# Kernel tuning notes

Hardware: AMD Instinct MI355X
Metric: run time of the kernel (lower is better)

The kernel has to match this reference:

```python
import jax, jax.numpy as jnp
import numpy as np

B, T, D, F, E, K = 2, 1024, 1024, 2048, 8, 2

def setup_inputs() -> dict:
    key = jax.random.key(0)
    ks = jax.random.split(key, 9)
    s = 0.02
    return {
        "states": jax.random.normal(ks[0], (B, T, D), dtype=jnp.float32),
        "Wg": jax.random.normal(ks[1], (D, E), dtype=jnp.float32) * s,
        "W_in": jax.random.normal(ks[2], (E, D, F), dtype=jnp.float32) * s,
        "b_in": jnp.zeros((E, F), dtype=jnp.float32),
        "W_scale": jax.random.normal(ks[3], (E, D, F), dtype=jnp.float32) * s,
        "b_scale": jnp.zeros((E, F), dtype=jnp.float32),
        "W_out": jax.random.normal(ks[4], (E, F, D), dtype=jnp.float32) * s,
        "b_out": jnp.zeros((E, D), dtype=jnp.float32),
        "num_selected": K,
    }

def reference(states, Wg, W_in, b_in, W_scale, b_scale, W_out, b_out, num_selected):
    b, t, d = states.shape
    x = states.reshape(-1, d)                      # [N, D]
    n = x.shape[0]
    # router: softmax over experts, then top-k + renormalize
    probs = jax.nn.softmax(x @ Wg, axis=-1)        # [N, E]
    topw, topi = jax.lax.top_k(probs, num_selected)  # [N, K]
    topw = topw / topw.sum(axis=-1, keepdims=True)
    # dense combine weights [N, E]: zero except selected experts
    w_full = jnp.zeros_like(probs).at[jnp.arange(n)[:, None], topi].set(topw)
    # gated-GELU expert MLPs, batched over experts
    h = jnp.einsum('nd,edf->enf', x, W_in) + b_in[:, None, :]       # [E, N, F]
    s = jnp.einsum('nd,edf->enf', x, W_scale) + b_scale[:, None, :]
    inner = jax.nn.gelu(h, approximate=False) * s                    # exact GELU (torch default)
    y = jnp.einsum('enf,efd->end', inner, W_out) + b_out[:, None, :]  # [E, N, D]
    out = jnp.einsum('end,ne->nd', y, w_full)                         # weighted combine
    return out.reshape(b, t, d)
```

## Files before the change

### kernel.cpp

```cpp
#include <hip/hip_runtime.h>
#include <hip/hip_bf16.h>
#include <math.h>

#define N_TOK 2048
#define DIM   1024
#define FF    2048
#define NEXP  8
#define NSLOT (N_TOK * 2)

typedef __attribute__((ext_vector_type(8))) short short8;
typedef __attribute__((ext_vector_type(4))) float f32x4;
typedef _Float16 half_t;
typedef __attribute__((ext_vector_type(4))) _Float16 h16x4;

__device__ __forceinline__ unsigned short f2bf(float f) {
    unsigned int u = __float_as_uint(f);
    u += 0x7FFFu + ((u >> 16) & 1u);
    return (unsigned short)(u >> 16);
}

#define GLOAD_LDS16(g, l) \
    __builtin_amdgcn_global_load_lds((const __attribute__((address_space(1))) unsigned int*)(g), \
                                     (__attribute__((address_space(3))) unsigned int*)(l), 16, 0, 0)

__global__ __launch_bounds__(256) void k_router(const float* __restrict__ x,
        const float* __restrict__ Wg, int* __restrict__ hdr,
        int* __restrict__ tok_e, float* __restrict__ tok_w) {
    int wave = threadIdx.x >> 6, lane = threadIdx.x & 63;
    int t = blockIdx.x * 4 + wave;
    float acc[NEXP];
#pragma unroll
    for (int e = 0; e < NEXP; ++e) acc[e] = 0.f;
    const float* xr = x + (size_t)t * DIM;
    for (int d = lane; d < DIM; d += 64) {
        float xv = xr[d];
        const float* wr = Wg + d * NEXP;
#pragma unroll
        for (int e = 0; e < NEXP; ++e) acc[e] += xv * wr[e];
    }
#pragma unroll
    for (int off = 32; off > 0; off >>= 1) {
#pragma unroll
        for (int e = 0; e < NEXP; ++e) acc[e] += __shfl_down(acc[e], off);
    }
    if (lane == 0) {
        int e0 = 0;
#pragma unroll
        for (int e = 1; e < NEXP; ++e) if (acc[e] > acc[e0]) e0 = e;
        int e1 = -1;
#pragma unroll
        for (int e = 0; e < NEXP; ++e) {
            if (e == e0) continue;
            if (e1 < 0 || acc[e] > acc[e1]) e1 = e;
        }
        float w0 = 1.f / (1.f + expf(acc[e1] - acc[e0]));
        tok_e[2 * t] = e0; tok_e[2 * t + 1] = e1;
        tok_w[2 * t] = w0; tok_w[2 * t + 1] = 1.f - w0;
        atomicAdd(&hdr[e0], 1);
        atomicAdd(&hdr[e1], 1);
    }
}

__global__ void k_scan(int* hdr) {
    if (threadIdx.x == 0 && blockIdx.x == 0) {
        int s = 0;
        for (int e = 0; e < NEXP; ++e) {
            hdr[16 + e] = s;
            hdr[8 + e]  = s;
            s += hdr[e];
        }
        hdr[24] = s;
    }
}

__global__ __launch_bounds__(256) void k_assign(const float* __restrict__ x,
        int* __restrict__ hdr, const int* __restrict__ tok_e,
        int* __restrict__ tok_slot, unsigned short* __restrict__ xg) {
    __shared__ int sh[2];
    int t = blockIdx.x;
    if (threadIdx.x == 0) {
        int e0 = tok_e[2 * t], e1 = tok_e[2 * t + 1];
        int p0 = atomicAdd(&hdr[8 + e0], 1);
        int p1 = atomicAdd(&hdr[8 + e1], 1);
        tok_slot[2 * t] = p0; tok_slot[2 * t + 1] = p1;
        sh[0] = p0; sh[1] = p1;
    }
    __syncthreads();
    int s0 = sh[0], s1 = sh[1];
    const float4* xr = (const float4*)(x + (size_t)t * DIM);
    float4 v = xr[threadIdx.x];
    ushort4 b;
    b.x = f2bf(v.x); b.y = f2bf(v.y); b.z = f2bf(v.z); b.w = f2bf(v.w);
    ((ushort4*)(xg + (size_t)s0 * DIM))[threadIdx.x] = b;
    ((ushort4*)(xg + (size_t)s1 * DIM))[threadIdx.x] = b;
}

__global__ __launch_bounds__(256) void k_cvt(
        const float* __restrict__ s0, const float* __restrict__ s1,
        const float* __restrict__ s2, unsigned short* __restrict__ d0,
        unsigned short* __restrict__ d1, unsigned short* __restrict__ d2) {
    int bz = blockIdx.y;
    int which = bz >> 3, e = bz & 7;
    int R = (which == 2) ? FF : DIM;
    int C = (which == 2) ? DIM : FF;
    const float* S = ((which == 0) ? s0 : (which == 1) ? s1 : s2) + (size_t)e * DIM * FF;
    unsigned short* D = ((which == 0) ? d0 : (which == 1) ? d1 : d2) + (size_t)e * DIM * FF;
    int tilesx = C >> 6;
    int tx = blockIdx.x % tilesx, ty = blockIdx.x / tilesx;
    int c0 = tx * 64, r0 = ty * 64;
    __shared__ unsigned short sh[64][65];
    int t = threadIdx.x;
    int rr = t >> 4, cc = (t & 15) * 4;
#pragma unroll
    for (int j = 0; j < 4; ++j) {
        int r = rr + j * 16;
        float4 v = *(const float4*)(S + (size_t)(r0 + r) * C + c0 + cc);
        sh[r][cc + 0] = f2bf(v.x);
        sh[r][cc + 1] = f2bf(v.y);
        sh[r][cc + 2] = f2bf(v.z);
        sh[r][cc + 3] = f2bf(v.w);
    }
    __syncthreads();
    int oc = t >> 2, orr = (t & 3) * 16;
    unsigned short tmp[16];
#pragma unroll
    for (int j = 0; j < 16; ++j) tmp[j] = sh[orr + j][oc];
    unsigned short* q = D + (size_t)(c0 + oc) * R + r0 + orr;
    *(uint4*)q       = *(uint4*)&tmp[0];
    *(uint4*)(q + 8) = *(uint4*)&tmp[8];
}

__global__ __launch_bounds__(256, 2) void k_expert_hs(
        const unsigned short* __restrict__ xg,
        const unsigned short* __restrict__ Wth,
        const unsigned short* __restrict__ Wts,
        const float* __restrict__ b_in, const float* __restrict__ b_sc,
        const int* __restrict__ hdr, unsigned short* __restrict__ inner) {
    int e = blockIdx.z;
    int cnt = hdr[e];
    int mtile = blockIdx.y;
    if (mtile * 128 >= cnt) return;
    int base = hdr[16 + e];
    int f0 = blockIdx.x * 128;

    __shared__ unsigned short As[128 * 32];
    __shared__ unsigned short Bh[128 * 32];
    __shared__ unsigned short Bs[128 * 32];

    int tid = threadIdx.x;
    int wave = tid >> 6, lane = tid & 63;
    int lr = lane & 15, lq = lane >> 4;
    int wm = (wave >> 1) * 64, wf = (wave & 1) * 64;

    f32x4 acch[4][4], accs[4][4];
#pragma unroll
    for (int mi = 0; mi < 4; ++mi)
#pragma unroll
        for (int fi = 0; fi < 4; ++fi) {
            acch[mi][fi] = (f32x4){0.f, 0.f, 0.f, 0.f};
            accs[mi][fi] = (f32x4){0.f, 0.f, 0.f, 0.f};
        }

    int swzc = (lane & 3) ^ ((lane >> 3) & 3);
    int goff = (lane >> 2) * DIM + swzc * 8;
    int rdo = lr * 32 + (lq ^ ((lr >> 1) & 3)) * 8;

    const unsigned short* Abase = xg  + (size_t)(base + mtile * 128) * DIM + goff;
    const unsigned short* Hbase = Wth + ((size_t)e * FF + f0) * DIM + goff;
    const unsigned short* Sbase = Wts + ((size_t)e * FF + f0) * DIM + goff;
    int p0 = wave * 32, p1 = wave * 32 + 16;

    for (int k0 = 0; k0 < DIM; k0 += 32) {
        __syncthreads();
        GLOAD_LDS16(Abase + (size_t)p0 * DIM + k0, &As[p0 * 32]);
        GLOAD_LDS16(Abase + (size_t)p1 * DIM + k0, &As[p1 * 32]);
        GLOAD_LDS16(Hbase + (size_t)p0 * DIM + k0, &Bh[p0 * 32]);
        GLOAD_LDS16(Hbase + (size_t)p1 * DIM + k0, &Bh[p1 * 32]);
        GLOAD_LDS16(Sbase + (size_t)p0 * DIM + k0, &Bs[p0 * 32]);
        GLOAD_LDS16(Sbase + (size_t)p1 * DIM + k0, &Bs[p1 * 32]);
        __syncthreads();

        short8 af[4], bhf[4], bsf[4];
#pragma unroll
        for (int mi = 0; mi < 4; ++mi)
            af[mi] = *(const short8*)&As[(wm + mi * 16) * 32 + rdo];
#pragma unroll
        for (int fi = 0; fi < 4; ++fi) {
            bhf[fi] = *(const short8*)&Bh[(wf + fi * 16) * 32 + rdo];
            bsf[fi] = *(const short8*)&Bs[(wf + fi * 16) * 32 + rdo];
        }
#pragma unroll
        for (int mi = 0; mi < 4; ++mi)
#pragma unroll
            for (int fi = 0; fi < 4; ++fi) {
                acch[mi][fi] = __builtin_amdgcn_mfma_f32_16x16x32_bf16(
                    af[mi], bhf[fi], acch[mi][fi], 0, 0, 0);
                accs[mi][fi] = __builtin_amdgcn_mfma_f32_16x16x32_bf16(
                    af[mi], bsf[fi], accs[mi][fi], 0, 0, 0);
            }
    }

#pragma unroll
    for (int fi = 0; fi < 4; ++fi) {
        int f = f0 + wf + fi * 16 + lr;
        float bi = b_in[e * FF + f];
        float bs2 = b_sc[e * FF + f];
#pragma unroll
        for (int mi = 0; mi < 4; ++mi) {
#pragma unroll
            for (int r = 0; r < 4; ++r) {
                int rl = wm + mi * 16 + lq * 4 + r;
                int grow = mtile * 128 + rl;
                if (grow < cnt) {
                    float h = acch[mi][fi][r] + bi;
                    float s = accs[mi][fi][r] + bs2;
                    float g = 0.5f * h * (1.f + erff(h * 0.70710678f));
                    inner[(size_t)(base + grow) * FF + f] = f2bf(g * s);
                }
            }
        }
    }
}

__global__ __launch_bounds__(256, 2) void k_expert_out(
        const unsigned short* __restrict__ inner,
        const unsigned short* __restrict__ Wto,
        const int* __restrict__ hdr, half_t* __restrict__ pbuf) {
    int e = blockIdx.z & 7;
    int ks = blockIdx.z >> 3;
    int cnt = hdr[e];
    int mtile = blockIdx.y;
    if (mtile * 128 >= cnt) return;
    int base = hdr[16 + e];
    int d0 = blockIdx.x * 256;

    __shared__ unsigned short As[128 * 32];
    __shared__ unsigned short Bt[256 * 32];

    int tid = threadIdx.x;
    int wave = tid >> 6, lane = tid & 63;
    int lr = lane & 15, lq = lane >> 4;
    int wm = (wave >> 1) * 64, wn = (wave & 1) * 128;

    f32x4 acc[4][8];
#pragma unroll
    for (int mi = 0; mi < 4; ++mi)
#pragma unroll
        for (int ni = 0; ni < 8; ++ni) acc[mi][ni] = (f32x4){0.f, 0.f, 0.f, 0.f};

    int swzc = (lane & 3) ^ ((lane >> 3) & 3);
    int goff = (lane >> 2) * FF + swzc * 8;
    int rdo = lr * 32 + (lq ^ ((lr >> 1) & 3)) * 8;

    const unsigned short* Abase = inner + (size_t)(base + mtile * 128) * FF + goff;
    const unsigned short* Bbase = Wto + ((size_t)e * DIM + d0) * FF + goff;
    int pa0 = wave * 32, pa1 = wave * 32 + 16;
    int pb0 = wave * 64;

    int kbeg = ks * (FF / 2), kend = kbeg + FF / 2;

    for (int k0 = kbeg; k0 < kend; k0 += 32) {
        __syncthreads();
        GLOAD_LDS16(Abase + (size_t)pa0 * FF + k0, &As[pa0 * 32]);
        GLOAD_LDS16(Abase + (size_t)pa1 * FF + k0, &As[pa1 * 32]);
#pragma unroll
        for (int j = 0; j < 4; ++j)
            GLOAD_LDS16(Bbase + (size_t)(pb0 + j * 16) * FF + k0, &Bt[(pb0 + j * 16) * 32]);
        __syncthreads();

        short8 af[4], bfm[8];
#pragma unroll
        for (int mi = 0; mi < 4; ++mi)
            af[mi] = *(const short8*)&As[(wm + mi * 16) * 32 + rdo];
#pragma unroll
        for (int ni = 0; ni < 8; ++ni)
            bfm[ni] = *(const short8*)&Bt[(wn + ni * 16) * 32 + rdo];
#pragma unroll
        for (int mi = 0; mi < 4; ++mi)
#pragma unroll
            for (int ni = 0; ni < 8; ++ni)
                acc[mi][ni] = __builtin_amdgcn_mfma_f32_16x16x32_bf16(
                    af[mi], bfm[ni], acc[mi][ni], 0, 0, 0);
    }

    half_t* P = pbuf + (size_t)ks * NSLOT * DIM;
#pragma unroll
    for (int ni = 0; ni < 8; ++ni) {
        int d = d0 + wn + ni * 16 + lr;
#pragma unroll
        for (int mi = 0; mi < 4; ++mi) {
#pragma unroll
            for (int r = 0; r < 4; ++r) {
                int rl = wm + mi * 16 + lq * 4 + r;
                int grow = mtile * 128 + rl;
                if (grow < cnt)
                    P[(size_t)(base + grow) * DIM + d] = (half_t)acc[mi][ni][r];
            }
        }
    }
}

__global__ __launch_bounds__(256) void k_combine(const half_t* __restrict__ pbuf,
        const int* __restrict__ tok_slot, const int* __restrict__ tok_e,
        const float* __restrict__ tok_w, const float* __restrict__ b_out,
        float* __restrict__ out) {
    int t = blockIdx.x;
    int d = threadIdx.x * 4;
    int s0 = tok_slot[2 * t], s1 = tok_slot[2 * t + 1];
    int e0 = tok_e[2 * t], e1 = tok_e[2 * t + 1];
    float w0 = tok_w[2 * t], w1 = tok_w[2 * t + 1];
    const half_t* pA = pbuf;
    const half_t* pB = pbuf + (size_t)NSLOT * DIM;
    h16x4 a0 = *(const h16x4*)&pA[(size_t)s0 * DIM + d];
    h16x4 a1 = *(const h16x4*)&pB[(size_t)s0 * DIM + d];
    h16x4 c0 = *(const h16x4*)&pA[(size_t)s1 * DIM + d];
    h16x4 c1 = *(const h16x4*)&pB[(size_t)s1 * DIM + d];
    float4 b0 = *(const float4*)&b_out[e0 * DIM + d];
    float4 b1 = *(const float4*)&b_out[e1 * DIM + d];
    float4 r;
    r.x = w0 * ((float)a0.x + (float)a1.x + b0.x) + w1 * ((float)c0.x + (float)c1.x + b1.x);
    r.y = w0 * ((float)a0.y + (float)a1.y + b0.y) + w1 * ((float)c0.y + (float)c1.y + b1.y);
    r.z = w0 * ((float)a0.z + (float)a1.z + b0.z) + w1 * ((float)c0.z + (float)c1.z + b1.z);
    r.w = w0 * ((float)a0.w + (float)a1.w + b0.w) + w1 * ((float)c0.w + (float)c1.w + b1.w);
    *(float4*)&out[(size_t)t * DIM + d] = r;
}

extern "C" void kernel_launch(void* const* d_in, const int* in_sizes, int n_in,
                              void* d_out, int out_size, void* d_ws, size_t ws_size,
                              hipStream_t stream) {
    (void)in_sizes; (void)n_in; (void)out_size; (void)ws_size;
    const float* x    = (const float*)d_in[0];
    const float* Wg   = (const float*)d_in[1];
    const float* Win  = (const float*)d_in[2];
    const float* b_in = (const float*)d_in[3];
    const float* Wsc  = (const float*)d_in[4];
    const float* b_sc = (const float*)d_in[5];
    const float* Wout = (const float*)d_in[6];
    const float* b_out= (const float*)d_in[7];
    float* out = (float*)d_out;

    char* ws = (char*)d_ws;
    int*   hdr      = (int*)ws;
    int*   tok_e    = (int*)(ws + 256);
    float* tok_w    = (float*)(ws + 16640);
    int*   tok_slot = (int*)(ws + 33024);
    unsigned short* xg    = (unsigned short*)(ws + 65792);
    unsigned short* inner = (unsigned short*)(ws + 65792 + 8388608);
    half_t* pbuf = (half_t*)(ws + 65792 + 8388608 + 16777216);
    unsigned short* wt_h = (unsigned short*)(ws + 65792 + 8388608 + 16777216 + 16777216);
    unsigned short* wt_s = wt_h + (size_t)NEXP * FF * DIM;
    unsigned short* wt_o = wt_s + (size_t)NEXP * FF * DIM;

    hipMemsetAsync(hdr, 0, 256, stream);
    k_cvt<<<dim3(512, 24), dim3(256), 0, stream>>>(Win, Wsc, Wout, wt_h, wt_s, wt_o);
    k_router<<<dim3(N_TOK / 4), dim3(256), 0, stream>>>(x, Wg, hdr, tok_e, tok_w);
    k_scan<<<dim3(1), dim3(64), 0, stream>>>(hdr);
    k_assign<<<dim3(N_TOK), dim3(256), 0, stream>>>(x, hdr, tok_e, tok_slot, xg);
    k_expert_hs<<<dim3(FF / 128, 16, NEXP), dim3(256), 0, stream>>>(xg, wt_h, wt_s, b_in, b_sc, hdr, inner);
    k_expert_out<<<dim3(DIM / 256, 16, NEXP * 2), dim3(256), 0, stream>>>(inner, wt_o, hdr, pbuf);
    k_combine<<<dim3(N_TOK), dim3(256), 0, stream>>>(pbuf, tok_slot, tok_e, tok_w, b_out, out);
}
```

Measured before the change: 457.3 us.

## Double-buffer LDS tiles in expert GEMM kernels to overlap loads with MFMA

Both expert GEMM kernels now use two LDS buffers per operand. The next K-slice is issued with global_load_lds before the current slice is computed, and one barrier per iteration replaces two. The aim is to hide global-memory latency behind MFMA work. LDS use doubles to about 48KB per block in each kernel, which may limit occupancy. The barrier alone may not guarantee the async LDS loads have completed, since no explicit vmcnt wait is added.

```diff
diff --git a/kernel.cpp b/kernel.cpp
--- a/kernel.cpp
+++ b/kernel.cpp
@@ -143,9 +143,9 @@
     int base = hdr[16 + e];
     int f0 = blockIdx.x * 128;
 
-    __shared__ unsigned short As[128 * 32];
-    __shared__ unsigned short Bh[128 * 32];
-    __shared__ unsigned short Bs[128 * 32];
+    __shared__ unsigned short As[2 * 128 * 32];
+    __shared__ unsigned short Bh[2 * 128 * 32];
+    __shared__ unsigned short Bs[2 * 128 * 32];
 
     int tid = threadIdx.x;
     int wave = tid >> 6, lane = tid & 63;
@@ -170,24 +170,36 @@
     const unsigned short* Sbase = Wts + ((size_t)e * FF + f0) * DIM + goff;
     int p0 = wave * 32, p1 = wave * 32 + 16;
 
-    for (int k0 = 0; k0 < DIM; k0 += 32) {
-        __syncthreads();
-        GLOAD_LDS16(Abase + (size_t)p0 * DIM + k0, &As[p0 * 32]);
-        GLOAD_LDS16(Abase + (size_t)p1 * DIM + k0, &As[p1 * 32]);
-        GLOAD_LDS16(Hbase + (size_t)p0 * DIM + k0, &Bh[p0 * 32]);
-        GLOAD_LDS16(Hbase + (size_t)p1 * DIM + k0, &Bh[p1 * 32]);
-        GLOAD_LDS16(Sbase + (size_t)p0 * DIM + k0, &Bs[p0 * 32]);
-        GLOAD_LDS16(Sbase + (size_t)p1 * DIM + k0, &Bs[p1 * 32]);
-        __syncthreads();
+    GLOAD_LDS16(Abase + (size_t)p0 * DIM, &As[p0 * 32]);
+    GLOAD_LDS16(Abase + (size_t)p1 * DIM, &As[p1 * 32]);
+    GLOAD_LDS16(Hbase + (size_t)p0 * DIM, &Bh[p0 * 32]);
+    GLOAD_LDS16(Hbase + (size_t)p1 * DIM, &Bh[p1 * 32]);
+    GLOAD_LDS16(Sbase + (size_t)p0 * DIM, &Bs[p0 * 32]);
+    GLOAD_LDS16(Sbase + (size_t)p1 * DIM, &Bs[p1 * 32]);
+    __syncthreads();
+
+    const int NSTEP = DIM / 32;
+    for (int t = 0; t < NSTEP; ++t) {
+        int co = (t & 1) * (128 * 32);
+        if (t + 1 < NSTEP) {
+            int no = ((t & 1) ^ 1) * (128 * 32);
+            int k1 = (t + 1) * 32;
+            GLOAD_LDS16(Abase + (size_t)p0 * DIM + k1, &As[no + p0 * 32]);
+            GLOAD_LDS16(Abase + (size_t)p1 * DIM + k1, &As[no + p1 * 32]);
+            GLOAD_LDS16(Hbase + (size_t)p0 * DIM + k1, &Bh[no + p0 * 32]);
+            GLOAD_LDS16(Hbase + (size_t)p1 * DIM + k1, &Bh[no + p1 * 32]);
+            GLOAD_LDS16(Sbase + (size_t)p0 * DIM + k1, &Bs[no + p0 * 32]);
+            GLOAD_LDS16(Sbase + (size_t)p1 * DIM + k1, &Bs[no + p1 * 32]);
+        }
 
         short8 af[4], bhf[4], bsf[4];
 #pragma unroll
         for (int mi = 0; mi < 4; ++mi)
-            af[mi] = *(const short8*)&As[(wm + mi * 16) * 32 + rdo];
+            af[mi] = *(const short8*)&As[co + (wm + mi * 16) * 32 + rdo];
 #pragma unroll
         for (int fi = 0; fi < 4; ++fi) {
-            bhf[fi] = *(const short8*)&Bh[(wf + fi * 16) * 32 + rdo];
-            bsf[fi] = *(const short8*)&Bs[(wf + fi * 16) * 32 + rdo];
+            bhf[fi] = *(const short8*)&Bh[co + (wf + fi * 16) * 32 + rdo];
+            bsf[fi] = *(const short8*)&Bs[co + (wf + fi * 16) * 32 + rdo];
         }
 #pragma unroll
         for (int mi = 0; mi < 4; ++mi)
@@ -198,6 +210,7 @@
                 accs[mi][fi] = __builtin_amdgcn_mfma_f32_16x16x32_bf16(
                     af[mi], bsf[fi], accs[mi][fi], 0, 0, 0);
             }
+        __syncthreads();
     }
 
 #pragma unroll
@@ -234,8 +247,8 @@
     int base = hdr[16 + e];
     int d0 = blockIdx.x * 256;
 
-    __shared__ unsigned short As[128 * 32];
-    __shared__ unsigned short Bt[256 * 32];
+    __shared__ unsigned short As[2 * 128 * 32];
+    __shared__ unsigned short Bt[2 * 256 * 32];
 
     int tid = threadIdx.x;
     int wave = tid >> 6, lane = tid & 63;
@@ -257,30 +270,42 @@
     int pa0 = wave * 32, pa1 = wave * 32 + 16;
     int pb0 = wave * 64;
 
-    int kbeg = ks * (FF / 2), kend = kbeg + FF / 2;
-
-    for (int k0 = kbeg; k0 < kend; k0 += 32) {
-        __syncthreads();
-        GLOAD_LDS16(Abase + (size_t)pa0 * FF + k0, &As[pa0 * 32]);
-        GLOAD_LDS16(Abase + (size_t)pa1 * FF + k0, &As[pa1 * 32]);
-#pragma unroll
-        for (int j = 0; j < 4; ++j)
-            GLOAD_LDS16(Bbase + (size_t)(pb0 + j * 16) * FF + k0, &Bt[(pb0 + j * 16) * 32]);
-        __syncthreads();
+    int kbeg = ks * (FF / 2);
+
+    GLOAD_LDS16(Abase + (size_t)pa0 * FF + kbeg, &As[pa0 * 32]);
+    GLOAD_LDS16(Abase + (size_t)pa1 * FF + kbeg, &As[pa1 * 32]);
+#pragma unroll
+    for (int j = 0; j < 4; ++j)
+        GLOAD_LDS16(Bbase + (size_t)(pb0 + j * 16) * FF + kbeg, &Bt[(pb0 + j * 16) * 32]);
+    __syncthreads();
+
+    const int NSTEP = (FF / 2) / 32;
+    for (int t = 0; t < NSTEP; ++t) {
+        int coA = (t & 1) * (128 * 32), coB = (t & 1) * (256 * 32);
+        if (t + 1 < NSTEP) {
+            int noA = ((t & 1) ^ 1) * (128 * 32), noB = ((t & 1) ^ 1) * (256 * 32);
+            int k1 = kbeg + (t + 1) * 32;
+            GLOAD_LDS16(Abase + (size_t)pa0 * FF + k1, &As[noA + pa0 * 32]);
+            GLOAD_LDS16(Abase + (size_t)pa1 * FF + k1, &As[noA + pa1 * 32]);
+#pragma unroll
+            for (int j = 0; j < 4; ++j)
+                GLOAD_LDS16(Bbase + (size_t)(pb0 + j * 16) * FF + k1, &Bt[noB + (pb0 + j * 16) * 32]);
+        }
 
         short8 af[4], bfm[8];
 #pragma unroll
         for (int mi = 0; mi < 4; ++mi)
-            af[mi] = *(const short8*)&As[(wm + mi * 16) * 32 + rdo];
+            af[mi] = *(const short8*)&As[coA + (wm + mi * 16) * 32 + rdo];
 #pragma unroll
         for (int ni = 0; ni < 8; ++ni)
-            bfm[ni] = *(const short8*)&Bt[(wn + ni * 16) * 32 + rdo];
+            bfm[ni] = *(const short8*)&Bt[coB + (wn + ni * 16) * 32 + rdo];
 #pragma unroll
         for (int mi = 0; mi < 4; ++mi)
 #pragma unroll
             for (int ni = 0; ni < 8; ++ni)
                 acc[mi][ni] = __builtin_amdgcn_mfma_f32_16x16x32_bf16(
                     af[mi], bfm[ni], acc[mi][ni], 0, 0, 0);
+        __syncthreads();
     }
 
     half_t* P = pbuf + (size_t)ks * NSLOT * DIM;
```

New measurement: 470.1 us. 2.8% more time.
